# Optimization experiments

Measured on AMD Instinct MI355X. Metric: run time of the kernel, lower is better.

Reference implementation:

```python
import jax, jax.numpy as jnp
import numpy as np

K = 3      # kernel size
PAD = 1    # padding


def _conv(x, w, b=None):
    y = jax.lax.conv_general_dilated(
        x, w, window_strides=(1, 1), padding=((PAD, PAD), (PAD, PAD)),
        dimension_numbers=('NCHW', 'OIHW', 'NCHW'))
    if b is not None:
        y = y + b[None, :, None, None]
    return y


def _deform_conv2d(x, offset, mask, weight):
    # torchvision deform_conv2d with offset_groups == C (one offset pair per
    # input channel per kernel tap), stride=1, dilation=1, zero padding.
    B, C, H, W = x.shape
    KK = K * K
    off = offset.reshape(B, C, KK, 2, H, W)   # [...,0]=dy, [...,1]=dx
    dy, dx = off[:, :, :, 0], off[:, :, :, 1]
    m = mask.reshape(B, C, KK, H, W)

    ki = (jnp.arange(KK) // K).reshape(1, 1, KK, 1, 1).astype(x.dtype)
    kj = (jnp.arange(KK) % K).reshape(1, 1, KK, 1, 1).astype(x.dtype)
    gy = jnp.arange(H, dtype=x.dtype).reshape(1, 1, 1, H, 1)
    gx = jnp.arange(W, dtype=x.dtype).reshape(1, 1, 1, 1, W)
    py = dy + gy - PAD + ki   # sampling y coords, [B,C,KK,H,W]
    px = dx + gx - PAD + kj   # sampling x coords

    # torchvision: sample is zero unless -1 < p < size
    valid = (py > -1) & (py < H) & (px > -1) & (px < W)
    y0f = jnp.floor(py)
    x0f = jnp.floor(px)
    wy = py - y0f
    wx = px - x0f
    y0 = y0f.astype(jnp.int32)
    x0 = x0f.astype(jnp.int32)
    y1 = y0 + 1
    x1 = x0 + 1

    xf = x.reshape(B, C, H * W)

    def gather(yi, xi):
        inb = (yi >= 0) & (yi < H) & (xi >= 0) & (xi < W)
        yc = jnp.clip(yi, 0, H - 1)
        xc = jnp.clip(xi, 0, W - 1)
        idx = (yc * W + xc).reshape(B, C, -1)
        v = jnp.take_along_axis(xf, idx, axis=2).reshape(yi.shape)
        return jnp.where(inb, v, jnp.zeros((), x.dtype))

    val = ((1 - wy) * (1 - wx) * gather(y0, x0)
           + (1 - wy) * wx * gather(y0, x1)
           + wy * (1 - wx) * gather(y1, x0)
           + wy * wx * gather(y1, x1))
    samp = jnp.where(valid, val, jnp.zeros((), x.dtype)) * m   # [B,C,KK,H,W]

    O = weight.shape[0]
    return jnp.einsum('bckhw,ock->bohw', samp, weight.reshape(O, C, KK))


def setup_inputs() -> dict:
    key = jax.random.key(0)
    k1, k2, k3, k4, k5, k6 = jax.random.split(key, 6)
    B, C, O, H, W = 8, 64, 128, 64, 64
    KK = K * K
    x = jax.random.normal(k1, (B, C, H, W), dtype=jnp.float32)
    # offset conv: 2*C*KK output channels (module inits to 0; use small random
    # weights so the irregular sampling path is exercised)
    w_off = jax.random.normal(k2, (2 * C * KK, C, K, K), dtype=jnp.float32) * 0.05
    b_off = jnp.zeros((2 * C * KK,), dtype=jnp.float32)
    w_mod = jax.random.normal(k3, (C * KK, C, K, K), dtype=jnp.float32) * 0.05
    b_mod = jax.random.normal(k4, (C * KK,), dtype=jnp.float32) * 0.05
    w_conv = jax.random.normal(k5, (O, C, K, K), dtype=jnp.float32) / np.sqrt(C * KK)
    return {"x": x, "w_off": w_off, "b_off": b_off,
            "w_mod": w_mod, "b_mod": b_mod, "w_conv": w_conv}


def reference(x, w_off, b_off, w_mod, b_mod, w_conv):
    H, W = x.shape[2], x.shape[3]
    max_off = max(H, W) / 4.0
    offset = jnp.clip(_conv(x, w_off, b_off), -max_off, max_off)
    mask = _conv(x, w_mod, b_mod)
    return _deform_conv2d(x, offset, mask, w_conv)
```

## Files before the change

### kernel.cpp

```cpp
#include <hip/hip_runtime.h>
#include <cstddef>
#include <cstdint>

#define TCNT 256

namespace {
constexpr int CIN    = 64;
constexpr int COUT   = 128;
constexpr int HDIM   = 64;
constexpr int WDIM   = 64;
constexpr int HW     = HDIM * WDIM;
constexpr int KD     = CIN * 9;
constexpr int NOFF   = 2 * CIN * 9;
constexpr int NTOT   = NOFF + CIN * 9;
constexpr int NBATCH = 8;
constexpr int HXW    = 66;
constexpr int COPAD  = 1792;
constexpr int NGT    = COPAD / 16;
constexpr float MAXOFF = 16.0f;

constexpr size_t XT_ELEMS = (size_t)NBATCH * HXW * HXW * 64;
constexpr size_t WP_ELEMS = (size_t)18 * NGT * 512;
constexpr size_t WC_ELEMS = (size_t)18 * 8 * 512;
constexpr size_t OFF_XFH  = 0;
constexpr size_t OFF_WPH  = XT_ELEMS;
constexpr size_t OFF_WPL  = XT_ELEMS + WP_ELEMS;
constexpr size_t OFF_WCH  = XT_ELEMS + 2 * WP_ELEMS;
constexpr size_t FIXED_BYTES = (XT_ELEMS + 2 * WP_ELEMS + WC_ELEMS) * 2;
}

typedef __attribute__((ext_vector_type(8))) short    s16x8;
typedef __attribute__((ext_vector_type(8))) _Float16 f16x8;
typedef __attribute__((ext_vector_type(4))) float    f32x4;

__device__ __forceinline__ unsigned short f2h(float v) {
  _Float16 h = (_Float16)v;
  return __builtin_bit_cast(unsigned short, h);
}
__device__ __forceinline__ float h2f(unsigned short u) {
  return (float)__builtin_bit_cast(_Float16, u);
}

__global__ __launch_bounds__(TCNT) void prep_x(
    const float* __restrict__ x, unsigned short* __restrict__ xFh)
{
  const int b  = blockIdx.y;
  const int yy = blockIdx.x;
  const int t  = threadIdx.x;
  unsigned short* oh = xFh + ((size_t)(b * HXW + yy)) * HXW * 64;
  if (yy == 0 || yy == HXW - 1) {
    for (int lin = t; lin < HXW * 64; lin += TCNT) oh[lin] = 0;
    return;
  }
  __shared__ float tile[64][65];
  const int y = yy - 1;
  #pragma unroll
  for (int i = 0; i < 4; ++i) {
    const int f = t + TCNT * i;
    const int c = f >> 4, xq = f & 15;
    const float4 v =
        *(const float4*)(x + ((size_t)(b * 64 + c)) * HW + y * WDIM + xq * 4);
    tile[c][xq * 4 + 0] = v.x; tile[c][xq * 4 + 1] = v.y;
    tile[c][xq * 4 + 2] = v.z; tile[c][xq * 4 + 3] = v.w;
  }
  if (t < 128) {
    const int c = t & 63, xe = (t >> 6) ? (HXW - 1) * 64 : 0;
    oh[xe + c] = 0;
  }
  __syncthreads();
  const int xc = t >> 2, cg = (t & 3) * 16;
  s16x8 h0, h1;
  #pragma unroll
  for (int u = 0; u < 8; ++u) h0[u] = (short)f2h(tile[cg + u][xc]);
  #pragma unroll
  for (int u = 0; u < 8; ++u) h1[u] = (short)f2h(tile[cg + 8 + u][xc]);
  *(s16x8*)(oh + (xc + 1) * 64 + cg)     = h0;
  *(s16x8*)(oh + (xc + 1) * 64 + cg + 8) = h1;
}

__global__ __launch_bounds__(TCNT) void prep_w(
    const float* __restrict__ w_off, const float* __restrict__ w_mod,
    unsigned short* __restrict__ wF1h, unsigned short* __restrict__ wF1l)
{
  const int g  = blockIdx.x;
  const int hh = blockIdx.y;
  const int r  = hh >> 1, ks = hh & 1;
  const int t  = threadIdx.x;
  const size_t base = ((size_t)hh * NGT + g) * 512;
  #pragma unroll
  for (int q = 0; q < 2; ++q) {
    const int e = t + q * 256;
    const int l = e >> 3, f = e & 7;
    const int co = g * 16 + (l & 15);
    const int c  = ks * 32 + (l >> 4) * 8 + f;
    float v = 0.f;
    if (co < NOFF)      v = w_off[(size_t)co * KD + c * 9 + r];
    else if (co < NTOT) v = w_mod[(size_t)(co - NOFF) * KD + c * 9 + r];
    const unsigned short hb = f2h(v);
    wF1h[base + e] = hb;
    wF1l[base + e] = f2h(v - h2f(hb));
  }
}

__global__ __launch_bounds__(TCNT) void prep_wc(
    const float* __restrict__ w_conv, unsigned short* __restrict__ wF2)
{
  const int nt = blockIdx.x;
  const int hh = blockIdx.y;
  const int sc = hh >> 1, ks = hh & 1;
  const int t  = threadIdx.x;
  const size_t base = ((size_t)hh * 8 + nt) * 512;
  #pragma unroll
  for (int q = 0; q < 2; ++q) {
    const int e = t + q * 256;
    const int l = e >> 3, f = e & 7;
    const int o = nt * 16 + (l & 15);
    const int c = sc * 64 + ks * 32 + (l >> 4) * 8 + f;
    wF2[base + e] = f2h(w_conv[(size_t)o * KD + c]);
  }
}

__global__ __launch_bounds__(TCNT, 3) void dcn_stage1(
    const unsigned short* __restrict__ xFh,
    const unsigned short* __restrict__ wF1h, const unsigned short* __restrict__ wF1l,
    const float* __restrict__ b_off, const float* __restrict__ b_mod,
    float* __restrict__ ws, int b0, int nb)
{
  __shared__ unsigned short Ah[2][128][32];

  const int t      = threadIdx.x;
  const int Mchunk = nb * HW;
  const int p0  = blockIdx.x * 128;
  const int b   = b0 + (p0 >> 12);
  const int h0  = (p0 & (HW - 1)) >> 6;
  const int co0 = blockIdx.y * 128;

  const int s_row = t >> 1;
  const int s_kh  = t & 1;
  const int s_sw  = ((s_row >> 1) & 3) << 3;
  const int a_h   = h0 + (s_row >> 6);
  const int a_w   = s_row & 63;
  const unsigned short* xbh = xFh + (size_t)b * HXW * HXW * 64;

  const int wave = t >> 6, lane = t & 63;
  const int wm = wave >> 1, wn = wave & 1;
  const int lrow = lane & 15;
  const int lkh  = lane >> 4;
  const int gbase = (co0 >> 4) + wn * 4;

  f32x4 acc[4][4];
  #pragma unroll
  for (int m = 0; m < 4; ++m)
    #pragma unroll
    for (int n = 0; n < 4; ++n) acc[m][n] = (f32x4)0.f;

  s16x8 rE0, rE1, rO0, rO1;
  f16x8 wh[4], wl[4];

#define ALOAD(D0, D1, H)                                                     \
  {                                                                          \
    const int r_  = (H) >> 1;                                                \
    const int ks_ = (H) & 1;                                                 \
    const int ki_ = r_ / 3;                                                  \
    const int kj_ = r_ - 3 * ki_;                                            \
    const size_t aoff_ = ((size_t)((a_h + ki_) * HXW + (a_w + kj_))) * 64 +  \
                         ks_ * 32 + s_kh * 16;                               \
    D0 = *(const s16x8*)(xbh + aoff_);                                       \
    D1 = *(const s16x8*)(xbh + aoff_ + 8);                                   \
  }

#define AWRITE(S0, S1, SEL)                                                  \
  {                                                                          \
    const int c0_ = (s_kh * 16) ^ s_sw;                                      \
    const int c1_ = (s_kh * 16 + 8) ^ s_sw;                                  \
    *(s16x8*)&Ah[SEL][s_row][c0_] = S0;                                      \
    *(s16x8*)&Ah[SEL][s_row][c1_] = S1;                                      \
  }

#define WLOAD(H)                                                             \
  {                                                                          \
    _Pragma("unroll")                                                        \
    for (int n = 0; n < 4; ++n) {                                            \
      const size_t o_ = ((size_t)(H) * NGT + gbase + n) * 512 + lane * 8;    \
      wh[n] = *(const f16x8*)(wF1h + o_);                                    \
      wl[n] = *(const f16x8*)(wF1l + o_);                                    \
    }                                                                        \
  }

#define MFMA_P(SEL)                                                          \
  {                                                                          \
    f16x8 fa[4];                                                             \
    _Pragma("unroll")                                                        \
    for (int m = 0; m < 4; ++m) {                                            \
      const int row = wm * 64 + m * 16 + lrow;                               \
      const int col = (lkh * 8) ^ (((row >> 1) & 3) << 3);                   \
      fa[m] = *(const f16x8*)&Ah[SEL][row][col];                             \
    }                                                                        \
    _Pragma("unroll")                                                        \
    for (int n = 0; n < 4; ++n) {                                            \
      _Pragma("unroll")                                                      \
      for (int m = 0; m < 4; ++m) {                                          \
        acc[m][n] = __builtin_amdgcn_mfma_f32_16x16x32_f16(fa[m], wh[n], acc[m][n], 0, 0, 0); \
        acc[m][n] = __builtin_amdgcn_mfma_f32_16x16x32_f16(fa[m], wl[n], acc[m][n], 0, 0, 0); \
      }                                                                      \
    }                                                                        \
  }

  ALOAD(rE0, rE1, 0)
  WLOAD(0)
  AWRITE(rE0, rE1, 0)
  ALOAD(rO0, rO1, 1)
  __syncthreads();

  #pragma unroll 1
  for (int h = 0; h < 17; ++h) {
    MFMA_P(h & 1)
    WLOAD(h + 1)
    if ((h & 1) == 0) {
      AWRITE(rO0, rO1, 1)
      if (h < 16) ALOAD(rE0, rE1, h + 2)
    } else {
      AWRITE(rE0, rE1, 0)
      if (h < 16) ALOAD(rO0, rO1, h + 2)
    }
    __syncthreads();
  }
  MFMA_P(1)

  const bool isOff = (co0 < NOFF);
  #pragma unroll
  for (int n = 0; n < 4; ++n) {
    const int cog = co0 + wn * 64 + n * 16 + lrow;
    if (cog >= NTOT) continue;
    const float bias = isOff ? b_off[cog] : b_mod[cog - NOFF];
    float* oplane = ws + (size_t)cog * Mchunk;
    #pragma unroll
    for (int m = 0; m < 4; ++m) {
      f32x4 v = acc[m][n];
      float4 o;
      o.x = v[0] + bias; o.y = v[1] + bias; o.z = v[2] + bias; o.w = v[3] + bias;
      if (isOff) {
        o.x = fminf(MAXOFF, fmaxf(-MAXOFF, o.x));
        o.y = fminf(MAXOFF, fmaxf(-MAXOFF, o.y));
        o.z = fminf(MAXOFF, fmaxf(-MAXOFF, o.z));
        o.w = fminf(MAXOFF, fmaxf(-MAXOFF, o.w));
      }
      const int pb = p0 + wm * 64 + m * 16 + lkh * 4;
      *(float4*)(oplane + pb) = o;
    }
  }
#undef ALOAD
#undef AWRITE
#undef WLOAD
#undef MFMA_P
}

__global__ __launch_bounds__(TCNT, 4) void dcn_stage2(
    const float* __restrict__ x, const float* __restrict__ planes,
    const unsigned short* __restrict__ wF2,
    float* __restrict__ out, int b0, int nb)
{
  __shared__ unsigned short SH[2][32][64], SL[2][32][64];

  const int t      = threadIdx.x;
  const int Mchunk = nb * HW;
  const int pc0 = blockIdx.x * 32;
  const int b   = b0 + (pc0 >> 12);
  const int h   = (pc0 & (HW - 1)) >> 6;
  const int w0  = pc0 & 63;

  const int tpx = t & 31;
  const int tsg = t >> 5;
  const int a_swz = (tpx & 7) << 3;
  const float* ws_pix = planes + pc0 + tpx;
  const float* xb     = x + (size_t)b * CIN * HW;

  const int wave = t >> 6, lane = t & 63;
  const int lrow = lane & 15, lkh = lane >> 4;
  const int f_swz = (lrow & 7) << 3;

  f32x4 acc[2][2];
  #pragma unroll
  for (int m = 0; m < 2; ++m)
    #pragma unroll
    for (int n = 0; n < 2; ++n) acc[m][n] = (f32x4)0.f;

  float vals[8];
  f16x8 w4[4];

#define SAMPLE(SCC)                                                          \
  {                                                                          \
    _Pragma("unroll")                                                        \
    for (int j = 0; j < 8; ++j) {                                            \
      const int sl = tsg * 8 + j;                                            \
      const int s  = (SCC) * 64 + sl;                                        \
      const int c  = s / 9;                                                  \
      const int kk = s - c * 9;                                              \
      const int ki = kk / 3;                                                 \
      const int kj = kk - ki * 3;                                            \
      const float dy = ws_pix[(size_t)(2 * s)     * Mchunk];                 \
      const float dx = ws_pix[(size_t)(2 * s + 1) * Mchunk];                 \
      const float m  = ws_pix[(size_t)(NOFF + s)  * Mchunk];                 \
      const float py = dy + (float)(h + ki - 1);                             \
      const float px = dx + (float)(w0 + tpx + kj - 1);                      \
      const bool valid = (py > -1.f) && (py < (float)HDIM) &&                \
                         (px > -1.f) && (px < (float)WDIM);                  \
      const float y0f = floorf(py), x0f = floorf(px);                        \
      const float wy = py - y0f, wx = px - x0f;                              \
      const int y0 = (int)y0f, x0 = (int)x0f;                                \
      const float* plane = xb + c * HW;                                      \
      float v00 = 0.f, v01 = 0.f, v10 = 0.f, v11 = 0.f;                      \
      if ((unsigned)y0 < (unsigned)HDIM) {                                   \
        const float* row = plane + (y0 << 6);                                \
        if ((unsigned)x0       < (unsigned)WDIM) v00 = row[x0];              \
        if ((unsigned)(x0 + 1) < (unsigned)WDIM) v01 = row[x0 + 1];          \
      }                                                                      \
      if ((unsigned)(y0 + 1) < (unsigned)HDIM) {                             \
        const float* row = plane + ((y0 + 1) << 6);                          \
        if ((unsigned)x0       < (unsigned)WDIM) v10 = row[x0];              \
        if ((unsigned)(x0 + 1) < (unsigned)WDIM) v11 = row[x0 + 1];          \
      }                                                                      \
      const float val = (1.f - wy) * ((1.f - wx) * v00 + wx * v01)           \
                      + wy         * ((1.f - wx) * v10 + wx * v11);          \
      vals[j] = valid ? val * m : 0.f;                                       \
    }                                                                        \
  }

#define PACK(SEL)                                                            \
  {                                                                          \
    s16x8 h8, l8;                                                            \
    _Pragma("unroll")                                                        \
    for (int u = 0; u < 8; ++u) {                                            \
      const unsigned short hb = f2h(vals[u]);                                \
      h8[u] = (short)hb;                                                     \
      l8[u] = (short)f2h(vals[u] - h2f(hb));                                 \
    }                                                                        \
    const int col = (tsg * 8) ^ a_swz;                                       \
    *(s16x8*)&SH[SEL][tpx][col] = h8;                                        \
    *(s16x8*)&SL[SEL][tpx][col] = l8;                                        \
  }

#define W2LOAD(SCC)                                                          \
  {                                                                          \
    _Pragma("unroll")                                                        \
    for (int ks = 0; ks < 2; ++ks)                                           \
      _Pragma("unroll")                                                      \
      for (int n = 0; n < 2; ++n) {                                          \
        const size_t o_ = (((size_t)(SCC) * 2 + ks) * 8 + wave * 2 + n) * 512\
                          + lane * 8;                                        \
        w4[ks * 2 + n] = *(const f16x8*)(wF2 + o_);                          \
      }                                                                      \
  }

#define MFMA2(SEL)                                                           \
  {                                                                          \
    _Pragma("unroll")                                                        \
    for (int ks = 0; ks < 2; ++ks) {                                         \
      const int colb = (ks * 32 + lkh * 8) ^ f_swz;                          \
      f16x8 fah[2], fal[2];                                                  \
      _Pragma("unroll")                                                      \
      for (int m = 0; m < 2; ++m) {                                          \
        fah[m] = *(const f16x8*)&SH[SEL][m * 16 + lrow][colb];               \
        fal[m] = *(const f16x8*)&SL[SEL][m * 16 + lrow][colb];               \
      }                                                                      \
      _Pragma("unroll")                                                      \
      for (int n = 0; n < 2; ++n) {                                          \
        _Pragma("unroll")                                                    \
        for (int m = 0; m < 2; ++m) {                                        \
          acc[m][n] = __builtin_amdgcn_mfma_f32_16x16x32_f16(fah[m], w4[ks * 2 + n], acc[m][n], 0, 0, 0); \
          acc[m][n] = __builtin_amdgcn_mfma_f32_16x16x32_f16(fal[m], w4[ks * 2 + n], acc[m][n], 0, 0, 0); \
        }                                                                    \
      }                                                                      \
    }                                                                        \
  }

  SAMPLE(0)
  PACK(0)
  W2LOAD(0)
  __syncthreads();

  #pragma unroll 1
  for (int sc = 0; sc < 8; ++sc) {
    MFMA2(sc & 1)
    W2LOAD(sc + 1)
    SAMPLE(sc + 1)
    PACK((sc + 1) & 1)
    __syncthreads();
  }
  MFMA2(0)

  #pragma unroll
  for (int n = 0; n < 2; ++n) {
    const int o = wave * 32 + n * 16 + lrow;
    float* obase = out + ((size_t)(b * COUT + o)) * HW + h * WDIM + w0;
    #pragma unroll
    for (int m = 0; m < 2; ++m) {
      const int pxl = m * 16 + lkh * 4;
      f32x4 v = acc[m][n];
      *(float4*)(obase + pxl) = make_float4(v[0], v[1], v[2], v[3]);
    }
  }
#undef SAMPLE
#undef PACK
#undef W2LOAD
#undef MFMA2
}

extern "C" void kernel_launch(void* const* d_in, const int* in_sizes, int n_in,
                              void* d_out, int out_size, void* d_ws, size_t ws_size,
                              hipStream_t stream) {
  (void)in_sizes; (void)n_in; (void)out_size;
  const float* x      = (const float*)d_in[0];
  const float* w_off  = (const float*)d_in[1];
  const float* b_off  = (const float*)d_in[2];
  const float* w_mod  = (const float*)d_in[3];
  const float* b_mod  = (const float*)d_in[4];
  const float* w_conv = (const float*)d_in[5];
  float* out = (float*)d_out;

  unsigned short* wsu = (unsigned short*)d_ws;
  unsigned short* xFh  = wsu + OFF_XFH;
  unsigned short* wF1h = wsu + OFF_WPH;
  unsigned short* wF1l = wsu + OFF_WPL;
  unsigned short* wF2  = wsu + OFF_WCH;
  float* planes = (float*)((char*)d_ws + FIXED_BYTES);

  const size_t ws_per_batch = (size_t)NTOT * HW * sizeof(float);
  size_t avail = (ws_size > FIXED_BYTES) ? (ws_size - FIXED_BYTES) : 0;
  int nb = (int)(avail / ws_per_batch);
  if (nb < 1) nb = 1;
  if (nb > NBATCH) nb = NBATCH;

  prep_x<<<dim3(HXW, NBATCH), TCNT, 0, stream>>>(x, xFh);
  prep_w<<<dim3(NGT, 18), TCNT, 0, stream>>>(w_off, w_mod, wF1h, wF1l);
  prep_wc<<<dim3(8, 18), TCNT, 0, stream>>>(w_conv, wF2);

  for (int b0 = 0; b0 < NBATCH; b0 += nb) {
    const int cur = (NBATCH - b0 < nb) ? (NBATCH - b0) : nb;
    dim3 g1(cur * 32, 14);
    dcn_stage1<<<g1, TCNT, 0, stream>>>(xFh, wF1h, wF1l, b_off, b_mod,
                                        planes, b0, cur);
    dcn_stage2<<<cur * 128, TCNT, 0, stream>>>(x, planes, wF2, out, b0, cur);
  }
}
```

Measured before the change: 333.9 us.

## Double-buffer weight registers and overlap sampling loads with MFMA in stage2

The stage-2 main loop is unrolled by two, and the weight fragments are double-buffered in registers (w4A/w4B). The next chunk's weight loads and gather sampling are now issued before the current chunk's MFMAs, so memory latency can hide behind matrix work. The occupancy hint in launch_bounds is dropped from 4 to the default, letting the compiler use more registers. The risks are lower occupancy and register pressure from the extra buffers.

```diff
diff --git a/kernel.cpp b/kernel.cpp
--- a/kernel.cpp
+++ b/kernel.cpp
@@ -255,7 +255,7 @@
 #undef MFMA_P
 }
 
-__global__ __launch_bounds__(TCNT, 4) void dcn_stage2(
+__global__ __launch_bounds__(TCNT) void dcn_stage2(
     const float* __restrict__ x, const float* __restrict__ planes,
     const unsigned short* __restrict__ wF2,
     float* __restrict__ out, int b0, int nb)
@@ -286,7 +286,7 @@
     for (int n = 0; n < 2; ++n) acc[m][n] = (f32x4)0.f;
 
   float vals[8];
-  f16x8 w4[4];
+  f16x8 w4A[4], w4B[4];
 
 #define SAMPLE(SCC)                                                          \
   {                                                                          \
@@ -340,7 +340,7 @@
     *(s16x8*)&SL[SEL][tpx][col] = l8;                                        \
   }
 
-#define W2LOAD(SCC)                                                          \
+#define W2LOAD(DST, SCC)                                                     \
   {                                                                          \
     _Pragma("unroll")                                                        \
     for (int ks = 0; ks < 2; ++ks)                                           \
@@ -348,11 +348,11 @@
       for (int n = 0; n < 2; ++n) {                                          \
         const size_t o_ = (((size_t)(SCC) * 2 + ks) * 8 + wave * 2 + n) * 512\
                           + lane * 8;                                        \
-        w4[ks * 2 + n] = *(const f16x8*)(wF2 + o_);                          \
-      }                                                                      \
-  }
-
-#define MFMA2(SEL)                                                           \
+        DST[ks * 2 + n] = *(const f16x8*)(wF2 + o_);                         \
+      }                                                                      \
+  }
+
+#define MFMA2(SEL, WREG)                                                     \
   {                                                                          \
     _Pragma("unroll")                                                        \
     for (int ks = 0; ks < 2; ++ks) {                                         \
@@ -367,8 +367,8 @@
       for (int n = 0; n < 2; ++n) {                                          \
         _Pragma("unroll")                                                    \
         for (int m = 0; m < 2; ++m) {                                        \
-          acc[m][n] = __builtin_amdgcn_mfma_f32_16x16x32_f16(fah[m], w4[ks * 2 + n], acc[m][n], 0, 0, 0); \
-          acc[m][n] = __builtin_amdgcn_mfma_f32_16x16x32_f16(fal[m], w4[ks * 2 + n], acc[m][n], 0, 0, 0); \
+          acc[m][n] = __builtin_amdgcn_mfma_f32_16x16x32_f16(fah[m], WREG[ks * 2 + n], acc[m][n], 0, 0, 0); \
+          acc[m][n] = __builtin_amdgcn_mfma_f32_16x16x32_f16(fal[m], WREG[ks * 2 + n], acc[m][n], 0, 0, 0); \
         }                                                                    \
       }                                                                      \
     }                                                                        \
@@ -376,18 +376,24 @@
 
   SAMPLE(0)
   PACK(0)
-  W2LOAD(0)
+  W2LOAD(w4A, 0)
   __syncthreads();
 
   #pragma unroll 1
-  for (int sc = 0; sc < 8; ++sc) {
-    MFMA2(sc & 1)
-    W2LOAD(sc + 1)
-    SAMPLE(sc + 1)
-    PACK((sc + 1) & 1)
+  for (int it = 0; it < 4; ++it) {
+    const int sce = 2 * it;
+    W2LOAD(w4B, sce + 1)
+    SAMPLE(sce + 1)
+    MFMA2(0, w4A)
+    PACK(1)
     __syncthreads();
-  }
-  MFMA2(0)
+    W2LOAD(w4A, sce + 2)
+    SAMPLE(sce + 2)
+    MFMA2(1, w4B)
+    PACK(0)
+    __syncthreads();
+  }
+  MFMA2(0, w4A)
 
   #pragma unroll
   for (int n = 0; n < 2; ++n) {
```

New measurement: 303.1 us. 9.2% less time.
